# Kernel optimization log

Measured on AMD Instinct MI355X. Metric: run time of the kernel, lower is better.

Reference implementation:

```python
import jax, jax.numpy as jnp
import numpy as np

NEG = -1e30  # stand-in for -inf, safe for grads


def ctc_loss(log_probs, targets, input_lengths, target_lengths):
    """PyTorch-style CTC loss, blank=0, reduction='mean'.
    log_probs: [B, T, V] log-softmaxed; targets: [B, S] (values in [1, V)).
    """
    B, T, V = log_probs.shape
    S = targets.shape[1]
    L = 2 * S + 1  # extended label seq: blank-interleaved
    ext = jnp.zeros((B, L), jnp.int32).at[:, 1::2].set(targets.astype(jnp.int32))
    prev2 = jnp.pad(ext[:, :-2], ((0, 0), (2, 0)), constant_values=-1)
    skip = (ext != 0) & (ext != prev2)  # [B, L] allow alpha[l-2] transition
    barange = jnp.arange(B)[:, None]

    # t = 0 init
    lp0e = log_probs[:, 0, :][barange, ext]  # [B, L]
    alpha0 = jnp.full((B, L), NEG, log_probs.dtype)
    alpha0 = alpha0.at[:, 0].set(lp0e[:, 0]).at[:, 1].set(lp0e[:, 1])

    def step(alpha, xs):
        t, lp_t = xs  # lp_t: [B, V]
        lpe = lp_t[barange, ext]  # [B, L]
        a1 = jnp.pad(alpha[:, :-1], ((0, 0), (1, 0)), constant_values=NEG)
        a2 = jnp.pad(alpha[:, :-2], ((0, 0), (2, 0)), constant_values=NEG)
        a2 = jnp.where(skip, a2, NEG)
        new = lpe + jnp.logaddexp(jnp.logaddexp(alpha, a1), a2)
        # freeze alpha past each sequence's length
        new = jnp.where((t < input_lengths)[:, None], new, alpha)
        return new, None

    ts = jnp.arange(1, T)
    lps = jnp.swapaxes(log_probs, 0, 1)[1:]  # [T-1, B, V]
    alpha, _ = jax.lax.scan(step, alpha0, (ts, lps))

    tl = target_lengths.astype(jnp.int32)
    brange = jnp.arange(B)
    end = alpha[brange, 2 * tl]       # trailing blank
    end2 = alpha[brange, 2 * tl - 1]  # last label
    per = -jnp.logaddexp(end, end2)
    # reduction='mean': divide each loss by its target_length, then batch mean
    return jnp.mean(per / target_lengths.astype(per.dtype))


def setup_inputs() -> dict:
    key = jax.random.key(0)
    k1, k2, k3 = jax.random.split(key, 3)
    B, T, Fd, V, S = 32, 2048, 1024, 256, 256
    features = jax.random.normal(k1, (B, T, Fd), jnp.float32)
    W = jax.random.normal(k2, (V, Fd), jnp.float32) / np.sqrt(Fd)
    b = jnp.zeros((V,), jnp.float32)
    targets = jax.random.randint(k3, (B, S), 1, V)  # avoid blank=0
    input_lengths = jnp.full((B,), T, jnp.int32)
    target_lengths = jnp.full((B,), S, jnp.int32)
    return {"features": features, "W": W, "b": b, "targets": targets,
            "input_lengths": input_lengths, "target_lengths": target_lengths}


def reference(features, W, b, targets, input_lengths, target_lengths):
    # dropout is identity at inference; classifier then log_softmax in fp32
    logits = jnp.einsum('btf,vf->btv', features, W) + b
    log_probs = jax.nn.log_softmax(logits.astype(jnp.float32), axis=-1)
    return ctc_loss(log_probs, targets, input_lengths, target_lengths)
```

## Files before the change

### kernel.cpp

```cpp
#include <hip/hip_runtime.h>
#include <hip/hip_bf16.h>

using bf16x8 = __attribute__((ext_vector_type(8))) short;
using f32x4  = __attribute__((ext_vector_type(4))) float;

constexpr int Bn = 32;
constexpr int Tn = 2048;
constexpr int Fn = 1024;
constexpr int Vn = 256;
constexpr int Sn = 256;
constexpr int Ln = 2 * Sn + 1;
constexpr int Mn = Bn * Tn;
constexpr int G2P = 272;
constexpr int DQ = 16;

#define NEGF (-1e30f)

__device__ __forceinline__ float exp2fast(float x) { return __builtin_amdgcn_exp2f(x); }
__device__ __forceinline__ float log2fast(float x) { return __builtin_amdgcn_logf(x); }

__device__ __forceinline__ unsigned int cvt_pk_bf16(float lo, float hi) {
    unsigned int r;
    asm("v_cvt_pk_bf16_f32 %0, %1, %2" : "=v"(r) : "v"(lo), "v"(hi));
    return r;
}

__device__ __forceinline__ float lae2(float x, float y) {
    float m = fmaxf(x, y);
    float d = fminf(x, y) - m;
    return m + log2fast(1.0f + exp2fast(d));
}
__device__ __forceinline__ float lae3(float x, float y, float z) {
    float m  = fmaxf(fmaxf(x, y), z);
    float md = __builtin_amdgcn_fmed3f(x, y, z);
    float mn = fminf(fminf(x, y), z);
    return m + log2fast(1.0f + exp2fast(md - m) + exp2fast(mn - m));
}

__global__ __launch_bounds__(256) void wcvt(const float* __restrict__ W,
                                            unsigned short* __restrict__ Wb)
{
    const int idx = (blockIdx.x * 256 + threadIdx.x) * 4;
    float4 v = *reinterpret_cast<const float4*>(W + idx);
    uint2 p;
    p.x = cvt_pk_bf16(v.x, v.y);
    p.y = cvt_pk_bf16(v.z, v.w);
    *reinterpret_cast<uint2*>(Wb + idx) = p;
}

__global__ __launch_bounds__(512) void gemm_ctc(
    const float* __restrict__ A,
    const unsigned short* __restrict__ Wb,
    const float* __restrict__ bias,
    const int* __restrict__ targets,
    float* __restrict__ G2)
{
    __shared__ char smem[70144];
    unsigned short* sA = (unsigned short*)smem;
    unsigned short* sB = (unsigned short*)(smem + 16384);
    float* yL    = (float*)smem;
    float* sRedA = (float*)(smem + 66048);
    float* sRedB = (float*)(smem + 68096);

    const int tid  = threadIdx.x;
    const int wid  = tid >> 6, lane = tid & 63;
    const int quad = lane >> 4, c16 = lane & 15;
    const int m0 = blockIdx.x * 128;
    const int wm = (wid & 1) * 64;
    const int wn = (wid >> 1) * 64;

    f32x4 acc[4][4] = {};

    const int arow = tid >> 2;
    const int akq  = (tid & 3) << 4;
    const float* aPtr = A + (size_t)(m0 + arow) * Fn + akq;
    const int aswz = (arow & 7) << 4;
    char* sAbase = (char*)sA + arow * 128;
    const int ab0 = (akq * 2) ^ aswz;
    const int ab1 = (akq * 2 + 16) ^ aswz;

    const int wrow8 = lane >> 3;
    const int wcol  = ((lane & 7) << 4) ^ (wrow8 << 4);

    for (int k0 = 0; k0 < Fn; k0 += 64) {
        #pragma unroll
        for (int i = 0; i < 4; ++i) {
            const int rbase = wid * 32 + i * 8;
            const unsigned short* g = Wb + (size_t)(rbase + wrow8) * Fn + k0;
            __builtin_amdgcn_global_load_lds(
                (const __attribute__((address_space(1))) unsigned int*)((const char*)g + wcol),
                (__attribute__((address_space(3))) unsigned int*)((char*)sB + rbase * 128),
                16, 0, 0);
        }
        const float4* ap = reinterpret_cast<const float4*>(aPtr + k0);
        float4 av0 = ap[0], av1 = ap[1], av2 = ap[2], av3 = ap[3];
        uint4 p;
        p.x = cvt_pk_bf16(av0.x, av0.y); p.y = cvt_pk_bf16(av0.z, av0.w);
        p.z = cvt_pk_bf16(av1.x, av1.y); p.w = cvt_pk_bf16(av1.z, av1.w);
        *reinterpret_cast<uint4*>(sAbase + ab0) = p;
        p.x = cvt_pk_bf16(av2.x, av2.y); p.y = cvt_pk_bf16(av2.z, av2.w);
        p.z = cvt_pk_bf16(av3.x, av3.y); p.w = cvt_pk_bf16(av3.z, av3.w);
        *reinterpret_cast<uint4*>(sAbase + ab1) = p;
        __syncthreads();

        #pragma unroll
        for (int kh = 0; kh < 2; ++kh) {
            const int colq = kh * 64 + quad * 16;
            bf16x8 af[4], bf[4];
            #pragma unroll
            for (int mt = 0; mt < 4; ++mt) {
                const int r = wm + mt * 16 + c16;
                af[mt] = *reinterpret_cast<const bf16x8*>((const char*)sA + r * 128 + (colq ^ ((r & 7) << 4)));
            }
            #pragma unroll
            for (int nt = 0; nt < 4; ++nt) {
                const int r = wn + nt * 16 + c16;
                bf[nt] = *reinterpret_cast<const bf16x8*>((const char*)sB + r * 128 + (colq ^ ((r & 7) << 4)));
            }
            #pragma unroll
            for (int mt = 0; mt < 4; ++mt)
                #pragma unroll
                for (int nt = 0; nt < 4; ++nt)
                    acc[mt][nt] = __builtin_amdgcn_mfma_f32_16x16x32_bf16(af[mt], bf[nt], acc[mt][nt], 0, 0, 0);
        }
        __syncthreads();
    }

    const float L2E = 1.4426950408889634f;
    const int wng = wid >> 1;

    float bv[4];
    #pragma unroll
    for (int nt = 0; nt < 4; ++nt) bv[nt] = bias[wn + nt * 16 + c16];
    #pragma unroll
    for (int mt = 0; mt < 4; ++mt)
        #pragma unroll
        for (int nt = 0; nt < 4; ++nt)
            #pragma unroll
            for (int r = 0; r < 4; ++r)
                acc[mt][nt][r] += bv[nt];

    float rmx[4][4];
    #pragma unroll
    for (int mt = 0; mt < 4; ++mt)
        #pragma unroll
        for (int r = 0; r < 4; ++r) {
            float m = fmaxf(fmaxf(acc[mt][0][r], acc[mt][1][r]),
                            fmaxf(acc[mt][2][r], acc[mt][3][r]));
            #pragma unroll
            for (int off = 8; off >= 1; off >>= 1) m = fmaxf(m, __shfl_xor(m, off, 64));
            rmx[mt][r] = m;
        }
    if (c16 == 0) {
        #pragma unroll
        for (int mt = 0; mt < 4; ++mt)
            #pragma unroll
            for (int r = 0; r < 4; ++r)
                sRedA[(wm + mt * 16 + quad * 4 + r) * 4 + wng] = rmx[mt][r];
    }
    __syncthreads();

    float mL[4][4], sm[4][4];
    #pragma unroll
    for (int mt = 0; mt < 4; ++mt)
        #pragma unroll
        for (int r = 0; r < 4; ++r) {
            const int row = wm + mt * 16 + quad * 4 + r;
            float4 mp = ((const float4*)sRedA)[row];
            mL[mt][r] = fmaxf(fmaxf(mp.x, mp.y), fmaxf(mp.z, mp.w)) * L2E;
            float s = 0.0f;
            #pragma unroll
            for (int nt = 0; nt < 4; ++nt)
                s += exp2fast(fmaf(acc[mt][nt][r], L2E, -mL[mt][r]));
            #pragma unroll
            for (int off = 8; off >= 1; off >>= 1) s += __shfl_xor(s, off, 64);
            sm[mt][r] = s;
        }
    if (c16 == 0) {
        #pragma unroll
        for (int mt = 0; mt < 4; ++mt)
            #pragma unroll
            for (int r = 0; r < 4; ++r)
                sRedB[(wm + mt * 16 + quad * 4 + r) * 4 + wng] = sm[mt][r];
    }
    __syncthreads();

    float cr[4][4];
    #pragma unroll
    for (int mt = 0; mt < 4; ++mt)
        #pragma unroll
        for (int r = 0; r < 4; ++r) {
            const int row = wm + mt * 16 + quad * 4 + r;
            float4 sp = ((const float4*)sRedB)[row];
            cr[mt][r] = -(mL[mt][r] + log2fast((sp.x + sp.y) + (sp.z + sp.w)));
        }

    const int* tg = targets + (m0 >> 11) * Sn;
    const int rl = tid >> 3, c0 = tid & 7;
    #pragma unroll
    for (int h = 0; h < 2; ++h) {
        if ((wid & 1) == h) {
            #pragma unroll
            for (int mt = 0; mt < 4; ++mt)
                #pragma unroll
                for (int nt = 0; nt < 4; ++nt)
                    #pragma unroll
                    for (int r = 0; r < 4; ++r)
                        yL[(mt * 16 + quad * 4 + r) * 258 + wn + nt * 16 + c16] =
                            fmaf(acc[mt][nt][r], L2E, cr[mt][r]);
        }
        __syncthreads();
        {
            const size_t gbase = (size_t)(m0 + h * 64 + rl) * G2P;
            const float* yrow = yL + rl * 258;
            for (int k = 0; k < 33; ++k) {
                const int c = c0 + k * 8;
                if (c < 257) {
                    const int src = (c == 0) ? 0 : tg[c - 1];
                    G2[gbase + c] = yrow[src];
                }
            }
        }
        __syncthreads();
    }
}

__global__ __launch_bounds__(512) void ctc_alpha(
    const float* __restrict__ G2, const int* __restrict__ targets,
    const int* __restrict__ ilen, const int* __restrict__ tlen,
    float* __restrict__ loss_b)
{
    const int b = blockIdx.x, tid = threadIdx.x;
    const int w = tid >> 6, j = tid & 63;
    __shared__ float sAl[Ln];
    const float* __restrict__ Gb = G2 + (size_t)b * Tn * G2P;
    const int* tg = targets + b * Sn;
    const int len = ilen[b];
    const int tl  = tlen[b];

    const int own_lo = (w == 0) ? 0 : 64 * w + 2;
    const int own_hi = min(64 * w + 66, Ln);
    const int lbase  = 64 * w - 62 + 2 * j;
    const int l0 = lbase, l1 = lbase + 1;
    const int s_c = min(max(32 * w - 31 + j, 0), Sn - 1);

    const bool own0 = (l0 >= own_lo) && (l0 < own_hi);
    const bool own1 = (l1 >= own_lo) && (l1 < own_hi);
    const bool re0  = (l0 >= 0) && (l0 < Ln) && !own0;
    const bool re1  = (l1 >= 0) && (l1 < Ln) && !own1;
    bool sk1 = false;
    if (l1 >= 1 && l1 < Ln) { int s = l1 >> 1; sk1 = (s == 0) || (tg[s] != tg[s - 1]); }

    float a0, a1;
    {
        float bl0 = Gb[0];
        float od0 = Gb[1 + s_c];
        a0 = (l0 == 0) ? bl0 : NEGF;
        a1 = (l1 == 1) ? od0 : NEGF;
    }
    if (own0) sAl[l0] = a0;
    if (own1) sAl[l1] = a1;
    __syncthreads();
    if (re0) a0 = sAl[l0];
    if (re1) a1 = sAl[l1];
    __syncthreads();

    unsigned oB = G2P, oO = G2P + 1 + s_c;
    float plB[DQ], plO[DQ];
    #pragma unroll
    for (int d = 0; d < DQ; ++d) {
        plB[d] = Gb[oB]; plO[d] = Gb[oO];
        oB += G2P; oO += G2P;
    }

    const int NEGI = __float_as_int(NEGF);
    int t = 1;
    for (int chunk = 0; chunk < 64; ++chunk) {
        #pragma unroll
        for (int kk = 0; kk < 32; ++kk, ++t) {
            const int pidx = kk & (DQ - 1);
            float gb = plB[pidx], go = plO[pidx];
            plB[pidx] = Gb[oB]; plO[pidx] = Gb[oO];
            oB += G2P; oO += G2P;
            float p = __int_as_float(
                __builtin_amdgcn_update_dpp(NEGI, __float_as_int(a1), 0x138, 0xf, 0xf, false));
            if (t < len) {
                float z  = sk1 ? p : NEGF;
                float n0 = gb + lae2(a0, p);
                float n1 = go + lae3(a1, a0, z);
                a0 = n0; a1 = n1;
            }
        }
        if (own0) sAl[l0] = a0;
        if (own1) sAl[l1] = a1;
        __syncthreads();
        if (re0) a0 = sAl[l0];
        if (re1) a1 = sAl[l1];
        __syncthreads();
    }

    if (tid == 0) {
        float e1 = sAl[2 * tl];
        float e2 = sAl[2 * tl - 1];
        loss_b[b] = -0.6931471805599453f * lae2(e1, e2) / (float)tl;
    }
}

__global__ void final_reduce(const float* __restrict__ loss_b, float* __restrict__ out)
{
    const int lane = threadIdx.x;
    float v = (lane < Bn) ? loss_b[lane] : 0.0f;
    #pragma unroll
    for (int off = 32; off >= 1; off >>= 1) v += __shfl_xor(v, off, 64);
    if (lane == 0) out[0] = v * (1.0f / Bn);
}

extern "C" void kernel_launch(void* const* d_in, const int* in_sizes, int n_in,
                              void* d_out, int out_size, void* d_ws, size_t ws_size,
                              hipStream_t stream) {
    const float* feat = (const float*)d_in[0];
    const float* W    = (const float*)d_in[1];
    const float* bias = (const float*)d_in[2];
    const int* tgt    = (const int*)d_in[3];
    const int* il     = (const int*)d_in[4];
    const int* tl     = (const int*)d_in[5];
    float* out = (float*)d_out;

    char* ws = (char*)d_ws;
    float* G2 = (float*)ws;
    size_t g2b = (size_t)Mn * G2P * sizeof(float) + 32768;
    unsigned short* Wb = (unsigned short*)(ws + g2b);
    float* lossb = (float*)(ws + g2b + (size_t)Vn * Fn * sizeof(unsigned short));

    wcvt<<<(Vn * Fn) / 1024, 256, 0, stream>>>(W, Wb);
    gemm_ctc<<<Mn / 128, 512, 0, stream>>>(feat, Wb, bias, tgt, G2);
    ctc_alpha<<<Bn, 512, 0, stream>>>(G2, tgt, il, tl, lossb);
    final_reduce<<<1, 64, 0, stream>>>(lossb, out);
}
```

Before: 662.3 us.

## Split CTC recursion into forward/backward halves and double-buffer GEMM W tiles

Replaces the serial forward alpha recursion over all time steps with a forward pass over the first half and a backward (beta) pass over the second half, run as separate blocks, then combines them with a logsumexp per batch. This halves the serial dependency chain length and doubles the number of blocks working on the recursion. The GEMM also double-buffers W tiles and prefetches the next A tile to overlap loads with MFMA, and rewrites the gather store into G2 to use precomputed per-lane target indices. These add more shared memory, an extra combine kernel, and correctness risk in the backward boundary handling.

```diff
diff --git a/kernel.cpp b/kernel.cpp
--- a/kernel.cpp
+++ b/kernel.cpp
@@ -13,6 +13,7 @@
 constexpr int Mn = Bn * Tn;
 constexpr int G2P = 272;
 constexpr int DQ = 16;
+constexpr int ABP = 520;
 
 #define NEGF (-1e30f)
 
@@ -48,14 +49,14 @@
     *reinterpret_cast<uint2*>(Wb + idx) = p;
 }
 
-__global__ __launch_bounds__(512) void gemm_ctc(
+__global__ __launch_bounds__(512, 4) void gemm_ctc(
     const float* __restrict__ A,
     const unsigned short* __restrict__ Wb,
     const float* __restrict__ bias,
     const int* __restrict__ targets,
     float* __restrict__ G2)
 {
-    __shared__ char smem[70144];
+    __shared__ char smem[81920];
     unsigned short* sA = (unsigned short*)smem;
     unsigned short* sB = (unsigned short*)(smem + 16384);
     float* yL    = (float*)smem;
@@ -82,17 +83,20 @@
     const int wrow8 = lane >> 3;
     const int wcol  = ((lane & 7) << 4) ^ (wrow8 << 4);
 
-    for (int k0 = 0; k0 < Fn; k0 += 64) {
-        #pragma unroll
-        for (int i = 0; i < 4; ++i) {
-            const int rbase = wid * 32 + i * 8;
-            const unsigned short* g = Wb + (size_t)(rbase + wrow8) * Fn + k0;
-            __builtin_amdgcn_global_load_lds(
-                (const __attribute__((address_space(1))) unsigned int*)((const char*)g + wcol),
-                (__attribute__((address_space(3))) unsigned int*)((char*)sB + rbase * 128),
-                16, 0, 0);
-        }
-        const float4* ap = reinterpret_cast<const float4*>(aPtr + k0);
+#define ISSUE_W(K0, BUF)                                                        \
+    _Pragma("unroll")                                                           \
+    for (int i = 0; i < 4; ++i) {                                               \
+        const int rbase = wid * 32 + i * 8;                                     \
+        const unsigned short* g = Wb + (size_t)(rbase + wrow8) * Fn + (K0);     \
+        __builtin_amdgcn_global_load_lds(                                       \
+            (const __attribute__((address_space(1))) unsigned int*)((const char*)g + wcol), \
+            (__attribute__((address_space(3))) unsigned int*)((char*)sB + (BUF) * 32768 + rbase * 128), \
+            16, 0, 0);                                                          \
+    }
+
+    ISSUE_W(0, 0);
+    {
+        const float4* ap = reinterpret_cast<const float4*>(aPtr);
         float4 av0 = ap[0], av1 = ap[1], av2 = ap[2], av3 = ap[3];
         uint4 p;
         p.x = cvt_pk_bf16(av0.x, av0.y); p.y = cvt_pk_bf16(av0.z, av0.w);
@@ -101,8 +105,17 @@
         p.x = cvt_pk_bf16(av2.x, av2.y); p.y = cvt_pk_bf16(av2.z, av2.w);
         p.z = cvt_pk_bf16(av3.x, av3.y); p.w = cvt_pk_bf16(av3.z, av3.w);
         *reinterpret_cast<uint4*>(sAbase + ab1) = p;
-        __syncthreads();
-
+    }
+    __syncthreads();
+
+    for (int it = 0; it < 16; ++it) {
+        float4 an0, an1, an2, an3;
+        if (it < 15) {
+            ISSUE_W((it + 1) * 64, (it + 1) & 1);
+            const float4* ap = reinterpret_cast<const float4*>(aPtr + (it + 1) * 64);
+            an0 = ap[0]; an1 = ap[1]; an2 = ap[2]; an3 = ap[3];
+        }
+        const char* sBb = (const char*)sB + (it & 1) * 32768;
         #pragma unroll
         for (int kh = 0; kh < 2; ++kh) {
             const int colq = kh * 64 + quad * 16;
@@ -115,7 +128,7 @@
             #pragma unroll
             for (int nt = 0; nt < 4; ++nt) {
                 const int r = wn + nt * 16 + c16;
-                bf[nt] = *reinterpret_cast<const bf16x8*>((const char*)sB + r * 128 + (colq ^ ((r & 7) << 4)));
+                bf[nt] = *reinterpret_cast<const bf16x8*>(sBb + r * 128 + (colq ^ ((r & 7) << 4)));
             }
             #pragma unroll
             for (int mt = 0; mt < 4; ++mt)
@@ -124,7 +137,18 @@
                     acc[mt][nt] = __builtin_amdgcn_mfma_f32_16x16x32_bf16(af[mt], bf[nt], acc[mt][nt], 0, 0, 0);
         }
         __syncthreads();
-    }
+        if (it < 15) {
+            uint4 p;
+            p.x = cvt_pk_bf16(an0.x, an0.y); p.y = cvt_pk_bf16(an0.z, an0.w);
+            p.z = cvt_pk_bf16(an1.x, an1.y); p.w = cvt_pk_bf16(an1.z, an1.w);
+            *reinterpret_cast<uint4*>(sAbase + ab0) = p;
+            p.x = cvt_pk_bf16(an2.x, an2.y); p.y = cvt_pk_bf16(an2.z, an2.w);
+            p.z = cvt_pk_bf16(an3.x, an3.y); p.w = cvt_pk_bf16(an3.z, an3.w);
+            *reinterpret_cast<uint4*>(sAbase + ab1) = p;
+            __syncthreads();
+        }
+    }
+#undef ISSUE_W
 
     const float L2E = 1.4426950408889634f;
     const int wng = wid >> 1;
@@ -151,6 +175,7 @@
             for (int off = 8; off >= 1; off >>= 1) m = fmaxf(m, __shfl_xor(m, off, 64));
             rmx[mt][r] = m;
         }
+    __syncthreads();
     if (c16 == 0) {
         #pragma unroll
         for (int mt = 0; mt < 4; ++mt)
@@ -196,7 +221,13 @@
         }
 
     const int* tg = targets + (m0 >> 11) * Sn;
-    const int rl = tid >> 3, c0 = tid & 7;
+    int tgc[5];
+    #pragma unroll
+    for (int k = 0; k < 5; ++k) {
+        const int c = lane + (k << 6);
+        tgc[k] = (c == 0) ? 0 : ((c < 257) ? tg[c - 1] : 0);
+    }
+
     #pragma unroll
     for (int h = 0; h < 2; ++h) {
         if ((wid & 1) == h) {
@@ -210,86 +241,60 @@
                             fmaf(acc[mt][nt][r], L2E, cr[mt][r]);
         }
         __syncthreads();
-        {
-            const size_t gbase = (size_t)(m0 + h * 64 + rl) * G2P;
-            const float* yrow = yL + rl * 258;
-            for (int k = 0; k < 33; ++k) {
-                const int c = c0 + k * 8;
-                if (c < 257) {
-                    const int src = (c == 0) ? 0 : tg[c - 1];
-                    G2[gbase + c] = yrow[src];
-                }
-            }
-        }
-        __syncthreads();
-    }
-}
-
-__global__ __launch_bounds__(512) void ctc_alpha(
+        #pragma unroll
+        for (int rr = 0; rr < 8; ++rr) {
+            const int row = wid * 8 + rr;
+            const float* yrow = yL + row * 258;
+            float vals[5];
+            #pragma unroll
+            for (int k = 0; k < 5; ++k) vals[k] = yrow[tgc[k]];
+            float* gout = G2 + (size_t)(m0 + h * 64 + row) * G2P;
+            #pragma unroll
+            for (int k = 0; k < 4; ++k) gout[lane + (k << 6)] = vals[k];
+            if (lane == 0) gout[256] = vals[4];
+        }
+        __syncthreads();
+    }
+}
+
+__global__ __launch_bounds__(512) void ctc_fb(
     const float* __restrict__ G2, const int* __restrict__ targets,
     const int* __restrict__ ilen, const int* __restrict__ tlen,
-    float* __restrict__ loss_b)
+    float* __restrict__ abuf)
 {
-    const int b = blockIdx.x, tid = threadIdx.x;
+    const int blk = blockIdx.x;
+    const bool bwd = blk >= Bn;
+    const int b = bwd ? blk - Bn : blk;
+    const int tid = threadIdx.x;
     const int w = tid >> 6, j = tid & 63;
     __shared__ float sAl[Ln];
     const float* __restrict__ Gb = G2 + (size_t)b * Tn * G2P;
     const int* tg = targets + b * Sn;
     const int len = ilen[b];
     const int tl  = tlen[b];
-
-    const int own_lo = (w == 0) ? 0 : 64 * w + 2;
-    const int own_hi = min(64 * w + 66, Ln);
-    const int lbase  = 64 * w - 62 + 2 * j;
-    const int l0 = lbase, l1 = lbase + 1;
-    const int s_c = min(max(32 * w - 31 + j, 0), Sn - 1);
-
-    const bool own0 = (l0 >= own_lo) && (l0 < own_hi);
-    const bool own1 = (l1 >= own_lo) && (l1 < own_hi);
-    const bool re0  = (l0 >= 0) && (l0 < Ln) && !own0;
-    const bool re1  = (l1 >= 0) && (l1 < Ln) && !own1;
-    bool sk1 = false;
-    if (l1 >= 1 && l1 < Ln) { int s = l1 >> 1; sk1 = (s == 0) || (tg[s] != tg[s - 1]); }
-
-    float a0, a1;
-    {
-        float bl0 = Gb[0];
-        float od0 = Gb[1 + s_c];
-        a0 = (l0 == 0) ? bl0 : NEGF;
-        a1 = (l1 == 1) ? od0 : NEGF;
-    }
-    if (own0) sAl[l0] = a0;
-    if (own1) sAl[l1] = a1;
-    __syncthreads();
-    if (re0) a0 = sAl[l0];
-    if (re1) a1 = sAl[l1];
-    __syncthreads();
-
-    unsigned oB = G2P, oO = G2P + 1 + s_c;
-    float plB[DQ], plO[DQ];
-    #pragma unroll
-    for (int d = 0; d < DQ; ++d) {
-        plB[d] = Gb[oB]; plO[d] = Gb[oO];
-        oB += G2P; oO += G2P;
-    }
-
+    float* outp = abuf + (size_t)(bwd ? Bn + b : b) * ABP;
     const int NEGI = __float_as_int(NEGF);
-    int t = 1;
-    for (int chunk = 0; chunk < 64; ++chunk) {
-        #pragma unroll
-        for (int kk = 0; kk < 32; ++kk, ++t) {
-            const int pidx = kk & (DQ - 1);
-            float gb = plB[pidx], go = plO[pidx];
-            plB[pidx] = Gb[oB]; plO[pidx] = Gb[oO];
-            oB += G2P; oO += G2P;
-            float p = __int_as_float(
-                __builtin_amdgcn_update_dpp(NEGI, __float_as_int(a1), 0x138, 0xf, 0xf, false));
-            if (t < len) {
-                float z  = sk1 ? p : NEGF;
-                float n0 = gb + lae2(a0, p);
-                float n1 = go + lae3(a1, a0, z);
-                a0 = n0; a1 = n1;
-            }
+
+    if (!bwd) {
+        const int own_lo = (w == 0) ? 0 : 64 * w + 2;
+        const int own_hi = min(64 * w + 66, Ln);
+        const int lbase  = 64 * w - 62 + 2 * j;
+        const int l0 = lbase, l1 = lbase + 1;
+        const int s_c = min(max(32 * w - 31 + j, 0), Sn - 1);
+
+        const bool own0 = (l0 >= own_lo) && (l0 < own_hi);
+        const bool own1 = (l1 >= own_lo) && (l1 < own_hi);
+        const bool re0  = (l0 >= 0) && (l0 < Ln) && !own0;
+        const bool re1  = (l1 >= 0) && (l1 < Ln) && !own1;
+        bool sk1 = false;
+        if (l1 >= 1 && l1 < Ln) { int s = l1 >> 1; sk1 = (s == 0) || (tg[s] != tg[s - 1]); }
+
+        float a0, a1;
+        {
+            float bl0 = Gb[0];
+            float od0 = Gb[1 + s_c];
+            a0 = (l0 == 0) ? bl0 : NEGF;
+            a1 = (l1 == 1) ? od0 : NEGF;
         }
         if (own0) sAl[l0] = a0;
         if (own1) sAl[l1] = a1;
@@ -297,13 +302,127 @@
         if (re0) a0 = sAl[l0];
         if (re1) a1 = sAl[l1];
         __syncthreads();
-    }
-
-    if (tid == 0) {
-        float e1 = sAl[2 * tl];
-        float e2 = sAl[2 * tl - 1];
-        loss_b[b] = -0.6931471805599453f * lae2(e1, e2) / (float)tl;
-    }
+
+        unsigned oB = G2P, oO = G2P + 1 + s_c;
+        float plB[DQ], plO[DQ];
+        #pragma unroll
+        for (int d = 0; d < DQ; ++d) {
+            plB[d] = Gb[oB]; plO[d] = Gb[oO];
+            oB += G2P; oO += G2P;
+        }
+
+        int t = 1;
+        for (int chunk = 0; chunk < 32; ++chunk) {
+            #pragma unroll
+            for (int kk = 0; kk < 32; ++kk, ++t) {
+                const int pidx = kk & (DQ - 1);
+                float gb = plB[pidx], go = plO[pidx];
+                plB[pidx] = Gb[oB]; plO[pidx] = Gb[oO];
+                oB += G2P; oO += G2P;
+                float p = __int_as_float(__builtin_amdgcn_update_dpp(
+                    NEGI, __float_as_int(a1), 0x138, 0xf, 0xf, false));
+                if (t < len) {
+                    float z  = sk1 ? p : NEGF;
+                    float n0 = gb + lae2(a0, p);
+                    float n1 = go + lae3(a1, a0, z);
+                    a0 = n0; a1 = n1;
+                }
+            }
+            if (own0) sAl[l0] = a0;
+            if (own1) sAl[l1] = a1;
+            __syncthreads();
+            if (re0) a0 = sAl[l0];
+            if (re1) a1 = sAl[l1];
+            __syncthreads();
+        }
+        if (own0) outp[l0] = a0;
+        if (own1) outp[l1] = a1;
+    } else {
+        const int l0 = 64 * w + 2 * j;
+        const int l1 = l0 + 1;
+        const int s  = 32 * w + j;
+        const int s_c = min(s, Sn - 1);
+        const bool act0 = l0 < Ln, act1 = l1 < Ln;
+        const bool own0 = act0 && ((j < 32) || (l0 == Ln - 1));
+        const bool own1 = act1 && (j < 32);
+        const bool re0 = act0 && !own0, re1 = act1 && !own1;
+        bool skb = false;
+        if (s + 1 < Sn) skb = (tg[s + 1] != tg[s]);
+
+        float a0 = (act0 && l0 == 2 * tl)     ? 0.0f : NEGF;
+        float a1 = (act1 && l1 == 2 * tl - 1) ? 0.0f : NEGF;
+        if (own0) sAl[l0] = a0;
+        if (own1) sAl[l1] = a1;
+        __syncthreads();
+        if (re0) a0 = sAl[l0];
+        if (re1) a1 = sAl[l1];
+        __syncthreads();
+
+        unsigned oB = (unsigned)Tn * G2P;
+        unsigned oO = oB + 1 + s_c;
+        float plB[DQ], plO[DQ];
+        #pragma unroll
+        for (int d = 0; d < DQ; ++d) {
+            plB[d] = Gb[oB]; plO[d] = Gb[oO];
+            oB -= G2P; oO -= G2P;
+        }
+
+        int tt = Tn;
+        for (int chunk = 0; chunk < 32; ++chunk) {
+            #pragma unroll
+            for (int kk = 0; kk < 32; ++kk, --tt) {
+                const int pidx = kk & (DQ - 1);
+                float gb = plB[pidx], go = plO[pidx];
+                plB[pidx] = Gb[oB]; plO[pidx] = Gb[oO];
+                oB -= G2P; oO -= G2P;
+                if (tt < len) {
+                    float c0 = gb + a0;
+                    float c1 = go + a1;
+                    float d0 = __int_as_float(__builtin_amdgcn_update_dpp(
+                        NEGI, __float_as_int(c0), 0x130, 0xf, 0xf, false));
+                    float d1 = __int_as_float(__builtin_amdgcn_update_dpp(
+                        NEGI, __float_as_int(c1), 0x130, 0xf, 0xf, false));
+                    a0 = lae2(c0, c1);
+                    a1 = lae3(c1, d0, skb ? d1 : NEGF);
+                }
+            }
+            if (own0) sAl[l0] = a0;
+            if (own1) sAl[l1] = a1;
+            __syncthreads();
+            if (re0) a0 = sAl[l0];
+            if (re1) a1 = sAl[l1];
+            __syncthreads();
+        }
+        if (own0) outp[l0] = a0;
+        if (own1) outp[l1] = a1;
+    }
+}
+
+__global__ __launch_bounds__(64) void ctc_combine(
+    const float* __restrict__ abuf, const int* __restrict__ tlen,
+    float* __restrict__ loss_b)
+{
+    const int b = blockIdx.x, lane = threadIdx.x;
+    const float* ap = abuf + (size_t)b * ABP;
+    const float* bp = abuf + (size_t)(Bn + b) * ABP;
+    float x[9];
+    #pragma unroll
+    for (int k = 0; k < 9; ++k) {
+        const int l = lane + (k << 6);
+        x[k] = (l < Ln) ? (ap[l] + bp[l]) : NEGF;
+    }
+    float m = x[0];
+    #pragma unroll
+    for (int k = 1; k < 9; ++k) m = fmaxf(m, x[k]);
+    #pragma unroll
+    for (int off = 32; off >= 1; off >>= 1) m = fmaxf(m, __shfl_xor(m, off, 64));
+    float s = 0.0f;
+    #pragma unroll
+    for (int k = 0; k < 9; ++k) s += exp2fast(x[k] - m);
+    #pragma unroll
+    for (int off = 32; off >= 1; off >>= 1) s += __shfl_xor(s, off, 64);
+    if (lane == 0)
+        loss_b[b] = -0.6931471805599453f * (m + log2fast(s)) / (float)tlen[b];
 }
 
 __global__ void final_reduce(const float* __restrict__ loss_b, float* __restrict__ out)
@@ -330,10 +449,12 @@
     float* G2 = (float*)ws;
     size_t g2b = (size_t)Mn * G2P * sizeof(float) + 32768;
     unsigned short* Wb = (unsigned short*)(ws + g2b);
-    float* lossb = (float*)(ws + g2b + (size_t)Vn * Fn * sizeof(unsigned short));
+    float* abuf  = (float*)(ws + g2b + (size_t)Vn * Fn * sizeof(unsigned short));
+    float* lossb = abuf + 2 * Bn * ABP;
 
     wcvt<<<(Vn * Fn) / 1024, 256, 0, stream>>>(W, Wb);
     gemm_ctc<<<Mn / 128, 512, 0, stream>>>(feat, Wb, bias, tgt, G2);
-    ctc_alpha<<<Bn, 512, 0, stream>>>(G2, tgt, il, tl, lossb);
+    ctc_fb<<<2 * Bn, 512, 0, stream>>>(G2, tgt, il, tl, abuf);
+    ctc_combine<<<Bn, 64, 0, stream>>>(abuf, tl, lossb);
     final_reduce<<<1, 64, 0, stream>>>(lossb, out);
 }
```

After: 564.4 us. 1.17x faster.
